# Kernel optimization log

Measured on AMD Instinct MI355X. Metric: run time of the kernel, lower is better.

Reference implementation:

```python
import jax, jax.numpy as jnp
import numpy as np

HEADS = 4


def rel_to_abs(x):
    """Convert relative logits [..., L, 2L-1] to absolute [..., L, L].
    out[..., i, j] = x[..., i, j - i + L - 1]."""
    L = x.shape[-2]
    idx = jnp.arange(L)[None, :] - jnp.arange(L)[:, None] + (L - 1)  # [L, L]
    idx = jnp.broadcast_to(idx, x.shape[:-1] + (L,))
    return jnp.take_along_axis(x, idx, axis=-1)


def setup_inputs() -> dict:
    key = jax.random.key(0)
    ks = jax.random.split(key, 5)
    b, c, h, w = 2, 256, 64, 64
    dh = c // HEADS
    return {
        "x": jax.random.normal(ks[0], (b, c, h, w), jnp.float32),
        "w_qkv": jax.random.normal(ks[1], (3 * c, c), jnp.float32) / np.float32(np.sqrt(c)),
        "w_out": jax.random.normal(ks[2], (c, c), jnp.float32) / np.float32(np.sqrt(c)),
        "rel_height": jax.random.normal(ks[3], (2 * h - 1, dh), jnp.float32),
        "rel_width": jax.random.normal(ks[4], (2 * w - 1, dh), jnp.float32),
    }


def reference(x, w_qkv, w_out, rel_height, rel_width):
    b, c, h, w = x.shape
    dh = c // HEADS
    N = h * w
    scale = dh ** -0.5

    # 1x1 conv == per-pixel matmul over channels
    qkv = jnp.einsum('bchw,oc->bohw', x, w_qkv)  # [b, 3c, h, w]
    q, k, v = jnp.split(qkv, 3, axis=1)

    def to_heads(t):  # [b, c, h, w] -> [b, H, N, dh]
        return t.reshape(b, HEADS, dh, N).transpose(0, 1, 3, 2)

    q = to_heads(q) * scale
    k = to_heads(k)
    v = to_heads(v)

    # content-content scores over spatial positions
    content = jnp.einsum('bnid,bnjd->bnij', q, k)  # [b, H, N, N]

    q5 = q.reshape(b, HEADS, h, w, dh)  # [b, H, x, y, dh]
    # width relative logits: [b,H,x,y,2w-1] -> abs -> [b,H,x,y,jw]
    rw = rel_to_abs(jnp.einsum('bnxyd,rd->bnxyr', q5, rel_width))
    # height relative logits on transposed spatial: [b,H,y,x,2h-1] -> [b,H,y,x,jh]
    rh = rel_to_abs(jnp.einsum('bnyxd,rd->bnyxr', q5.transpose(0, 1, 3, 2, 4), rel_height))

    logits = content.reshape(b, HEADS, h, w, h, w)
    logits = logits + rw[:, :, :, :, None, :]  # broadcast width bias over target height jh
    logits = logits + rh.transpose(0, 1, 3, 2, 4)[:, :, :, :, :, None]  # [b,H,x,y,jh] over jw

    attn = jax.nn.softmax(logits.reshape(b, HEADS, N, N), axis=-1)
    out = jnp.einsum('bnij,bnjd->bnid', attn, v)  # [b, H, N, dh]
    out = out.transpose(0, 1, 3, 2).reshape(b, c, h, w)
    out = jnp.einsum('bchw,oc->bohw', out, w_out)  # 1x1 out projection
    return out + x
```

## Files before the change

kernel.cpp:

```cpp
#include <hip/hip_runtime.h>

typedef unsigned short u16;
typedef unsigned int u32;
typedef __bf16 bf16x8 __attribute__((ext_vector_type(8)));
typedef __bf16 bf16x2 __attribute__((ext_vector_type(2)));
typedef float f32x4 __attribute__((ext_vector_type(4)));
typedef float f32x2 __attribute__((ext_vector_type(2)));
typedef u32 u32x4 __attribute__((ext_vector_type(4)));
typedef u32 u32x2 __attribute__((ext_vector_type(2)));
typedef short s16x4 __attribute__((ext_vector_type(4)));

#define DEVI __device__ __forceinline__

#if defined(__has_builtin)
#if __has_builtin(__builtin_amdgcn_exp2f)
#define EXP2F(x) __builtin_amdgcn_exp2f(x)
#endif
#endif
#ifndef EXP2F
#define EXP2F(x) exp2f(x)
#endif

#define MFMA16(a, b, c) __builtin_amdgcn_mfma_f32_16x16x32_bf16(a, b, c, 0, 0, 0)
#define MFMA1K(a, b, c) __builtin_amdgcn_mfma_f32_16x16x16bf16_1k(a, b, c, 0, 0, 0)

DEVI u16 f2bf(float f) {
    u32 u = __builtin_bit_cast(u32, f);
    u = (u + 0x7FFFu + ((u >> 16) & 1u)) >> 16;
    return (u16)u;
}
DEVI float bf2f(u16 h) {
    u32 u = ((u32)h) << 16;
    return __builtin_bit_cast(float, u);
}
DEVI float bfhi(u32 u) { return __builtin_bit_cast(float, u & 0xFFFF0000u); }
DEVI float bflo(u32 u) { return __builtin_bit_cast(float, u << 16); }
DEVI bf16x8 bc8(u32x4 u) { return __builtin_bit_cast(bf16x8, u); }
DEVI u32 pack2(float a, float b) {
    f32x2 v = {a, b};
    bf16x2 h = __builtin_convertvector(v, bf16x2);
    return __builtin_bit_cast(u32, h);
}

#define QSCALE 0.18033688011112042f

__global__ __launch_bounds__(256) void k_prep(const float* __restrict__ x,
                                              const float* __restrict__ wq,
                                              const float* __restrict__ wo,
                                              const float* __restrict__ relh,
                                              const float* __restrict__ relw,
                                              u16* __restrict__ xt, u16* __restrict__ wqb,
                                              u16* __restrict__ wob, u16* __restrict__ relhb,
                                              u16* __restrict__ relwb) {
    int bid = blockIdx.x;
    int t = threadIdx.x;
    if (bid < 512) {
        int pm = bid & 63, cm = (bid >> 6) & 3, b = bid >> 8;
        int p0 = pm * 64, c0 = cm * 64;
        __shared__ float tile[64][65];
#pragma unroll
        for (int it = 0; it < 16; ++it) {
            int idx = it * 256 + t;
            int cl = idx >> 6, pl = idx & 63;
            tile[cl][pl] = x[((size_t)(b * 256 + c0 + cl)) * 4096 + p0 + pl];
        }
        __syncthreads();
#pragma unroll
        for (int it = 0; it < 16; ++it) {
            int idx = it * 256 + t;
            int pl = idx >> 6, cl = idx & 63;
            xt[((size_t)(b * 4096 + p0 + pl)) * 256 + c0 + cl] = f2bf(tile[cl][pl]);
        }
    } else {
        int i0 = (bid - 512) * 256 + t;
#pragma unroll
        for (int i = i0; i < 196608; i += 65536) wqb[i] = f2bf(wq[i]);
        if (i0 < 65536) wob[i0] = f2bf(wo[i0]);
        if (i0 < 8192) {
            relhb[i0] = (i0 < 8128) ? f2bf(relh[i0]) : (u16)0;
            relwb[i0] = (i0 < 8128) ? f2bf(relw[i0]) : (u16)0;
        }
    }
}

__global__ __launch_bounds__(256) void k_qkv(const u16* __restrict__ xt, const u16* __restrict__ wqb,
                                             const u16* __restrict__ relwb,
                                             const u16* __restrict__ relhb,
                                             u16* __restrict__ q, u16* __restrict__ k,
                                             u16* __restrict__ vt, u16* __restrict__ Wabs,
                                             u16* __restrict__ Habs) {
    int pm = blockIdx.x, on = blockIdx.y, b = blockIdx.z;
    int p0 = pm * 64, o0 = on * 64;
    __shared__ __align__(16) u16 Bt[64 * 264];
    int t = threadIdx.x;
    int wv = t >> 6, l = t & 63, quad = l >> 4, li = l & 15;

    u32x4 areg[8];
    const u32x4* arow = (const u32x4*)(xt + ((size_t)(b * 4096 + p0 + wv * 16 + li)) * 256);
#pragma unroll
    for (int kc = 0; kc < 8; ++kc) areg[kc] = arow[kc * 4 + quad];

    {
        int row = t >> 2, c0 = (t & 3) * 64;
        const u32x4* g = (const u32x4*)(wqb + (size_t)(o0 + row) * 256 + c0);
        u32x4* s = (u32x4*)(Bt + row * 264 + c0);
#pragma unroll
        for (int kk = 0; kk < 8; ++kk) s[kk] = g[kk];
    }
    __syncthreads();

    f32x4 acc[4] = {{0, 0, 0, 0}, {0, 0, 0, 0}, {0, 0, 0, 0}, {0, 0, 0, 0}};
#pragma unroll
    for (int kc = 0; kc < 8; ++kc) {
        bf16x8 a = bc8(areg[kc]);
#pragma unroll
        for (int ct = 0; ct < 4; ++ct) {
            bf16x8 bb = bc8(*(const u32x4*)(Bt + (ct * 16 + li) * 264 + kc * 32 + quad * 8));
            acc[ct] = MFMA16(a, bb, acc[ct]);
        }
    }

    int tensor = on >> 2, head = on & 3;
    if (tensor == 2) {
        __syncthreads();
        u16* T = Bt;
#pragma unroll
        for (int ct = 0; ct < 4; ++ct)
#pragma unroll
            for (int r = 0; r < 4; ++r)
                T[(ct * 16 + li) * 72 + wv * 16 + quad * 4 + r] = f2bf(acc[ct][r]);
        __syncthreads();
        int dr = t >> 2, pc = (t & 3) * 16;
        u32x4* g = (u32x4*)(vt + ((size_t)((b * 4 + head) * 64 + dr)) * 4096 + p0 + pc);
        const u32x4* s2 = (const u32x4*)(T + dr * 72 + pc);
        g[0] = s2[0];
        g[1] = s2[1];
    } else {
        u16* outp = (tensor == 0) ? q : k;
        float sc = (tensor == 0) ? QSCALE : 1.0f;
#pragma unroll
        for (int ct = 0; ct < 4; ++ct)
#pragma unroll
            for (int r = 0; r < 4; ++r) {
                int p = p0 + wv * 16 + quad * 4 + r;
                int d = ct * 16 + li;
                outp[((size_t)((b * 4 + head) * 4096 + p)) * 64 + d] = f2bf(acc[ct][r] * sc);
            }
        if (tensor == 0) {
            int bh = b * 4 + head;
            u16* T = Bt;
            u16* Ls = Bt + 64 * 72;
            __syncthreads();
#pragma unroll
            for (int ct = 0; ct < 4; ++ct)
#pragma unroll
                for (int r = 0; r < 4; ++r)
                    T[(wv * 16 + quad * 4 + r) * 72 + ct * 16 + li] = f2bf(acc[ct][r] * QSCALE);
            {
                int row = t >> 1, half = t & 1;
                const u32x4* g2 = (const u32x4*)(relwb + row * 64 + half * 32);
                u32x4* s2 = (u32x4*)(Ls + row * 72 + half * 32);
#pragma unroll
                for (int kk = 0; kk < 4; ++kk) s2[kk] = g2[kk];
            }
            __syncthreads();
            u32x4 aq2[2];
            aq2[0] = *(const u32x4*)(T + (wv * 16 + li) * 72 + quad * 8);
            aq2[1] = *(const u32x4*)(T + (wv * 16 + li) * 72 + 32 + quad * 8);

            f32x4 acc2[8];
#pragma unroll
            for (int ct = 0; ct < 8; ++ct) acc2[ct] = (f32x4){0.f, 0.f, 0.f, 0.f};
#pragma unroll
            for (int kc = 0; kc < 2; ++kc) {
                bf16x8 a = bc8(aq2[kc]);
#pragma unroll
                for (int ct = 0; ct < 8; ++ct) {
                    bf16x8 bb = bc8(*(const u32x4*)(Ls + (ct * 16 + li) * 72 + kc * 32 + quad * 8));
                    acc2[ct] = MFMA16(a, bb, acc2[ct]);
                }
            }
#pragma unroll
            for (int ct = 0; ct < 8; ++ct)
#pragma unroll
                for (int r = 0; r < 4; ++r) {
                    int row = wv * 16 + quad * 4 + r;
                    int j = (ct * 16 + li) - 63 + row;
                    if (j >= 0 && j < 64)
                        Wabs[((size_t)(bh * 4096 + p0 + row)) * 64 + j] = f2bf(acc2[ct][r]);
                }
            __syncthreads();
            {
                int row = t >> 1, half = t & 1;
                const u32x4* g2 = (const u32x4*)(relhb + row * 64 + half * 32);
                u32x4* s2 = (u32x4*)(Ls + row * 72 + half * 32);
#pragma unroll
                for (int kk = 0; kk < 4; ++kk) s2[kk] = g2[kk];
            }
            __syncthreads();
#pragma unroll
            for (int ct = 0; ct < 8; ++ct) acc2[ct] = (f32x4){0.f, 0.f, 0.f, 0.f};
#pragma unroll
            for (int kc = 0; kc < 2; ++kc) {
                bf16x8 a = bc8(aq2[kc]);
#pragma unroll
                for (int ct = 0; ct < 8; ++ct) {
                    bf16x8 bb = bc8(*(const u32x4*)(Ls + (ct * 16 + li) * 72 + kc * 32 + quad * 8));
                    acc2[ct] = MFMA16(a, bb, acc2[ct]);
                }
            }
#pragma unroll
            for (int ct = 0; ct < 8; ++ct)
#pragma unroll
                for (int r = 0; r < 4; ++r) {
                    int row = wv * 16 + quad * 4 + r;
                    int j = (ct * 16 + li) - 63 + pm;
                    if (j >= 0 && j < 64)
                        Habs[((size_t)(bh * 4096 + p0 + row)) * 64 + j] = f2bf(acc2[ct][r]);
                }
        }
    }
}

__global__ __launch_bounds__(256, 2) void k_flash(const u16* __restrict__ q,
                                                  const u16* __restrict__ kg,
                                                  const u16* __restrict__ vt,
                                                  const u16* __restrict__ Wabs,
                                                  const u16* __restrict__ Habs,
                                                  u16* __restrict__ OP,
                                                  float* __restrict__ LS) {
    int pm = blockIdx.x, bh = blockIdx.y, ks = blockIdx.z;
    int p0 = pm * 128;
    __shared__ __align__(16) u16 Kt[2][64 * 72];
    __shared__ __align__(16) u16 Vl[2][64 * 72];
    __shared__ __align__(16) u16 Hl[128 * 24];
    int t = threadIdx.x, wv = t >> 6, l = t & 63, quad = l >> 4, li = l & 15;
    int rbase = wv * 32;

    u32x4 aq[2][2];
#pragma unroll
    for (int rs = 0; rs < 2; ++rs) {
        const u32x4* qrow =
            (const u32x4*)(q + ((size_t)(bh * 4096 + p0 + rbase + rs * 16 + li)) * 64);
        aq[rs][0] = qrow[quad];
        aq[rs][1] = qrow[4 + quad];
    }

    f32x4 wb4[2][4];
#pragma unroll
    for (int rs = 0; rs < 2; ++rs)
#pragma unroll
        for (int ct = 0; ct < 4; ++ct) {
            const u32* wp = (const u32*)(Wabs +
                                         ((size_t)(bh * 4096 + p0 + rbase + rs * 16 + li)) * 64 +
                                         ct * 16 + quad * 4);
            u32 lo = wp[0], hi = wp[1];
            wb4[rs][ct] = (f32x4){bflo(lo), bfhi(lo), bflo(hi), bfhi(hi)};
        }

    {
        int row = t >> 1, half = t & 1;
        const u32x4* g =
            (const u32x4*)(Habs + ((size_t)(bh * 4096 + p0 + row)) * 64 + ks * 16 + half * 8);
        *(u32x4*)(Hl + row * 24 + half * 8) = g[0];
    }

    int srow = t >> 2, scc = (t & 3) * 16;
    {
        int j0 = ks * 1024;
        const u32x4* gk = (const u32x4*)(kg + ((size_t)(bh * 4096 + j0 + srow)) * 64 + scc);
        u32x4* sk = (u32x4*)(Kt[0] + srow * 72 + scc);
        sk[0] = gk[0];
        sk[1] = gk[1];
        const u32x4* gv = (const u32x4*)(vt + ((size_t)(bh * 64 + srow)) * 4096 + j0 + scc);
        u32x4* sv = (u32x4*)(Vl[0] + srow * 72 + scc);
        sv[0] = gv[0];
        sv[1] = gv[1];
    }

    f32x4 oacc[2][5];
#pragma unroll
    for (int rs = 0; rs < 2; ++rs)
#pragma unroll
        for (int ct = 0; ct < 5; ++ct) oacc[rs][ct] = (f32x4){0.f, 0.f, 0.f, 0.f};

    const s16x4 ones = {(short)0x3F80, (short)0x3F80, (short)0x3F80, (short)0x3F80};

    u32x4 kreg[2], vreg[2];
    for (int kt = 0; kt < 16; ++kt) {
        __syncthreads();
        int cur = kt & 1;
        const u16* Kc = Kt[cur];
        const u16* Vc = Vl[cur];
        if (kt < 15) {
            int j0 = (ks * 16 + kt + 1) * 64;
            const u32x4* gk = (const u32x4*)(kg + ((size_t)(bh * 4096 + j0 + srow)) * 64 + scc);
            kreg[0] = gk[0];
            kreg[1] = gk[1];
            const u32x4* gv = (const u32x4*)(vt + ((size_t)(bh * 64 + srow)) * 4096 + j0 + scc);
            vreg[0] = gv[0];
            vreg[1] = gv[1];
        }

        float hh0 = bf2f(Hl[(rbase + li) * 24 + kt]);
        float hh1 = bf2f(Hl[(rbase + 16 + li) * 24 + kt]);
        f32x4 s[2][4];
#pragma unroll
        for (int ct = 0; ct < 4; ++ct) {
            s[0][ct] = wb4[0][ct] + hh0;
            s[1][ct] = wb4[1][ct] + hh1;
        }
#pragma unroll
        for (int kc = 0; kc < 2; ++kc) {
            bf16x8 b0 = bc8(aq[0][kc]), b1 = bc8(aq[1][kc]);
#pragma unroll
            for (int ct = 0; ct < 4; ++ct) {
                bf16x8 af = bc8(*(const u32x4*)(Kc + (ct * 16 + li) * 72 + kc * 32 + quad * 8));
                s[0][ct] = MFMA16(af, b0, s[0][ct]);
                s[1][ct] = MFMA16(af, b1, s[1][ct]);
            }
        }

        s16x4 pf[2][4];
#pragma unroll
        for (int rs = 0; rs < 2; ++rs)
#pragma unroll
            for (int ct = 0; ct < 4; ++ct) {
                u32x2 pp;
                pp.x = pack2(EXP2F(s[rs][ct][0]), EXP2F(s[rs][ct][1]));
                pp.y = pack2(EXP2F(s[rs][ct][2]), EXP2F(s[rs][ct][3]));
                pf[rs][ct] = __builtin_bit_cast(s16x4, pp);
            }

#pragma unroll
        for (int jt = 0; jt < 4; ++jt) {
            s16x4 a0 = pf[0][jt], a1 = pf[1][jt];
#pragma unroll
            for (int dt = 0; dt < 4; ++dt) {
                s16x4 bv = __builtin_bit_cast(
                    s16x4, *(const u32x2*)(Vc + (dt * 16 + li) * 72 + jt * 16 + quad * 4));
                oacc[0][dt] = MFMA1K(a0, bv, oacc[0][dt]);
                oacc[1][dt] = MFMA1K(a1, bv, oacc[1][dt]);
            }
            oacc[0][4] = MFMA1K(a0, ones, oacc[0][4]);
            oacc[1][4] = MFMA1K(a1, ones, oacc[1][4]);
        }

        if (kt < 15) {
            u32x4* sk = (u32x4*)(Kt[cur ^ 1] + srow * 72 + scc);
            sk[0] = kreg[0];
            sk[1] = kreg[1];
            u32x4* sv = (u32x4*)(Vl[cur ^ 1] + srow * 72 + scc);
            sv[0] = vreg[0];
            sv[1] = vreg[1];
        }
    }

#pragma unroll
    for (int rs = 0; rs < 2; ++rs) {
#pragma unroll
        for (int ct = 0; ct < 4; ++ct)
#pragma unroll
            for (int r = 0; r < 4; ++r) {
                int p = p0 + rbase + rs * 16 + quad * 4 + r;
                OP[((size_t)((ks * 8 + bh) * 4096 + p)) * 64 + ct * 16 + li] =
                    f2bf(oacc[rs][ct][r]);
            }
        if (li == 0) {
#pragma unroll
            for (int r = 0; r < 4; ++r) {
                int p = p0 + rbase + rs * 16 + quad * 4 + r;
                LS[(size_t)(ks * 8 + bh) * 4096 + p] = oacc[rs][4][r];
            }
        }
    }
}

__global__ __launch_bounds__(256) void k_out2(const u16* __restrict__ wob,
                                              const u16* __restrict__ OP,
                                              const float* __restrict__ LS,
                                              const float* __restrict__ x,
                                              float* __restrict__ out) {
    int pm = blockIdx.x, b = blockIdx.y, com = blockIdx.z;
    int p0 = pm * 64;
    __shared__ __align__(16) u16 Bt[64 * 264];
    int t = threadIdx.x, wv = t >> 6, l = t & 63, quad = l >> 4, li = l & 15;

    {
        int row = t >> 2, head = t & 3;
        int bh = b * 4 + head;
        int p = p0 + row;
        const u32x4* op[4];
        float lsum = 0.f;
#pragma unroll
        for (int s2 = 0; s2 < 4; ++s2) {
            op[s2] = (const u32x4*)(OP + ((size_t)((s2 * 8 + bh) * 4096 + p)) * 64);
            lsum += LS[(size_t)(s2 * 8 + bh) * 4096 + p];
        }
        float linv = 1.0f / lsum;
        u16* dst = Bt + row * 264 + head * 64;
#pragma unroll
        for (int kk = 0; kk < 8; ++kk) {
            u32x4 a = op[0][kk], c = op[1][kk], e = op[2][kk], f = op[3][kk];
            u32x4 pk;
            pk.x = pack2((bflo(a.x) + bflo(c.x) + bflo(e.x) + bflo(f.x)) * linv,
                         (bfhi(a.x) + bfhi(c.x) + bfhi(e.x) + bfhi(f.x)) * linv);
            pk.y = pack2((bflo(a.y) + bflo(c.y) + bflo(e.y) + bflo(f.y)) * linv,
                         (bfhi(a.y) + bfhi(c.y) + bfhi(e.y) + bfhi(f.y)) * linv);
            pk.z = pack2((bflo(a.z) + bflo(c.z) + bflo(e.z) + bflo(f.z)) * linv,
                         (bfhi(a.z) + bfhi(c.z) + bfhi(e.z) + bfhi(f.z)) * linv);
            pk.w = pack2((bflo(a.w) + bflo(c.w) + bflo(e.w) + bflo(f.w)) * linv,
                         (bfhi(a.w) + bfhi(c.w) + bfhi(e.w) + bfhi(f.w)) * linv);
            *(u32x4*)(dst + kk * 8) = pk;
        }
    }
    __syncthreads();

    int co0 = com * 64;
    f32x4 acc[4] = {{0, 0, 0, 0}, {0, 0, 0, 0}, {0, 0, 0, 0}, {0, 0, 0, 0}};
    const u32x4* arow = (const u32x4*)(wob + (size_t)(co0 + wv * 16 + li) * 256);
#pragma unroll
    for (int kc = 0; kc < 8; ++kc) {
        bf16x8 a = bc8(arow[kc * 4 + quad]);
#pragma unroll
        for (int ct = 0; ct < 4; ++ct) {
            bf16x8 bb = bc8(*(const u32x4*)(Bt + (ct * 16 + li) * 264 + kc * 32 + quad * 8));
            acc[ct] = MFMA16(a, bb, acc[ct]);
        }
    }
#pragma unroll
    for (int ct = 0; ct < 4; ++ct)
#pragma unroll
        for (int r = 0; r < 4; ++r) {
            size_t idx =
                ((size_t)(b * 256 + co0 + wv * 16 + quad * 4 + r)) * 4096 + p0 + ct * 16 + li;
            out[idx] = acc[ct][r] + x[idx];
        }
}

extern "C" void kernel_launch(void* const* d_in, const int* in_sizes, int n_in, void* d_out,
                              int out_size, void* d_ws, size_t ws_size, hipStream_t stream) {
    const float* x = (const float*)d_in[0];
    const float* wqkv = (const float*)d_in[1];
    const float* wout = (const float*)d_in[2];
    const float* relh = (const float*)d_in[3];
    const float* relw = (const float*)d_in[4];
    float* out = (float*)d_out;
    char* ws = (char*)d_ws;

    u16* xt = (u16*)(ws + 0);
    u16* wqb = (u16*)(ws + 4194304);
    u16* wob = (u16*)(ws + 4587520);
    u16* relwb = (u16*)(ws + 4718592);
    u16* relhb = (u16*)(ws + 4734976);
    u16* qb = (u16*)(ws + 4751360);
    u16* kb = (u16*)(ws + 8945664);
    u16* vtb = (u16*)(ws + 13139968);
    u16* Wabs = (u16*)(ws + 17334272);
    u16* Habs = (u16*)(ws + 21528576);
    u16* OPart = (u16*)(ws + 25722880);
    float* LSum = (float*)(ws + 0);

    k_prep<<<768, 256, 0, stream>>>(x, wqkv, wout, relh, relw, xt, wqb, wob, relhb, relwb);
    k_qkv<<<dim3(64, 12, 2), 256, 0, stream>>>(xt, wqb, relwb, relhb, qb, kb, vtb, Wabs, Habs);
    k_flash<<<dim3(32, 8, 4), 256, 0, stream>>>(qb, kb, vtb, Wabs, Habs, OPart, LSum);
    k_out2<<<dim3(64, 2, 4), 256, 0, stream>>>(wob, OPart, LSum, x, out);
}
```

Before: 153.6 us.

## Use direct global-to-LDS loads, transpose Habs layout, raise flash occupancy, merge out tiles

k_qkv now stages the weight tile with global_load_lds and an XOR/rotation swizzle instead of padded register copies. Habs is written transposed so k_flash can prefetch per-key-tile height biases straight into registers and drop its LDS staging buffer. k_flash launch bounds are raised to 4 blocks per SM. k_out2 computes two output-channel tiles per block, halving the grid and the repeated OP reduction. Risks: the strided transposed Habs writes are uncoalesced, and the higher occupancy may cause register spills.

After: 170.0 us. 1.11x slower.

```diff
diff --git a/kernel.cpp b/kernel.cpp
--- a/kernel.cpp
+++ b/kernel.cpp
@@ -23,6 +23,13 @@
 
 #define MFMA16(a, b, c) __builtin_amdgcn_mfma_f32_16x16x32_bf16(a, b, c, 0, 0, 0)
 #define MFMA1K(a, b, c) __builtin_amdgcn_mfma_f32_16x16x16bf16_1k(a, b, c, 0, 0, 0)
+
+typedef __attribute__((address_space(1))) u32 gu32;
+typedef __attribute__((address_space(3))) u32 lu32;
+DEVI void gll16(const u16* g, u16* l) {
+    __builtin_amdgcn_global_load_lds((const gu32*)g, (lu32*)l, 16, 0, 0);
+}
+#define WAIT_VM0() __builtin_amdgcn_s_waitcnt(0x0f70)
 
 DEVI u16 f2bf(float f) {
     u32 u = __builtin_bit_cast(u32, f);
@@ -88,10 +95,10 @@
                                              const u16* __restrict__ relhb,
                                              u16* __restrict__ q, u16* __restrict__ k,
                                              u16* __restrict__ vt, u16* __restrict__ Wabs,
-                                             u16* __restrict__ Habs) {
+                                             u16* __restrict__ HabsT) {
     int pm = blockIdx.x, on = blockIdx.y, b = blockIdx.z;
     int p0 = pm * 64, o0 = on * 64;
-    __shared__ __align__(16) u16 Bt[64 * 264];
+    __shared__ __align__(16) u16 Sm[64 * 256];
     int t = threadIdx.x;
     int wv = t >> 6, l = t & 63, quad = l >> 4, li = l & 15;
 
@@ -101,12 +108,15 @@
     for (int kc = 0; kc < 8; ++kc) areg[kc] = arow[kc * 4 + quad];
 
     {
-        int row = t >> 2, c0 = (t & 3) * 64;
-        const u32x4* g = (const u32x4*)(wqb + (size_t)(o0 + row) * 256 + c0);
-        u32x4* s = (u32x4*)(Bt + row * 264 + c0);
-#pragma unroll
-        for (int kk = 0; kk < 8; ++kk) s[kk] = g[kk];
-    }
+        int pc = l & 31;
+#pragma unroll
+        for (int i = 0; i < 8; ++i) {
+            int r = wv * 16 + i * 2 + (l >> 5);
+            gll16(wqb + (size_t)(o0 + r) * 256 + ((pc + r) & 31) * 8,
+                  Sm + (wv * 16 + i * 2) * 256);
+        }
+    }
+    WAIT_VM0();
     __syncthreads();
 
     f32x4 acc[4] = {{0, 0, 0, 0}, {0, 0, 0, 0}, {0, 0, 0, 0}, {0, 0, 0, 0}};
@@ -115,7 +125,8 @@
         bf16x8 a = bc8(areg[kc]);
 #pragma unroll
         for (int ct = 0; ct < 4; ++ct) {
-            bf16x8 bb = bc8(*(const u32x4*)(Bt + (ct * 16 + li) * 264 + kc * 32 + quad * 8));
+            bf16x8 bb = bc8(*(const u32x4*)(Sm + (ct * 16 + li) * 256 +
+                                            (((kc * 4 + quad) - (ct * 16 + li)) & 31) * 8));
             acc[ct] = MFMA16(a, bb, acc[ct]);
         }
     }
@@ -123,7 +134,7 @@
     int tensor = on >> 2, head = on & 3;
     if (tensor == 2) {
         __syncthreads();
-        u16* T = Bt;
+        u16* T = Sm;
 #pragma unroll
         for (int ct = 0; ct < 4; ++ct)
 #pragma unroll
@@ -148,8 +159,8 @@
             }
         if (tensor == 0) {
             int bh = b * 4 + head;
-            u16* T = Bt;
-            u16* Ls = Bt + 64 * 72;
+            u16* T = Sm;
+            u16* Ls = Sm + 64 * 72;
             __syncthreads();
 #pragma unroll
             for (int ct = 0; ct < 4; ++ct)
@@ -216,24 +227,23 @@
                     int row = wv * 16 + quad * 4 + r;
                     int j = (ct * 16 + li) - 63 + pm;
                     if (j >= 0 && j < 64)
-                        Habs[((size_t)(bh * 4096 + p0 + row)) * 64 + j] = f2bf(acc2[ct][r]);
+                        HabsT[((size_t)(bh * 64 + j)) * 4096 + p0 + row] = f2bf(acc2[ct][r]);
                 }
         }
     }
 }
 
-__global__ __launch_bounds__(256, 2) void k_flash(const u16* __restrict__ q,
+__global__ __launch_bounds__(256, 4) void k_flash(const u16* __restrict__ q,
                                                   const u16* __restrict__ kg,
                                                   const u16* __restrict__ vt,
                                                   const u16* __restrict__ Wabs,
-                                                  const u16* __restrict__ Habs,
+                                                  const u16* __restrict__ HabsT,
                                                   u16* __restrict__ OP,
                                                   float* __restrict__ LS) {
     int pm = blockIdx.x, bh = blockIdx.y, ks = blockIdx.z;
     int p0 = pm * 128;
     __shared__ __align__(16) u16 Kt[2][64 * 72];
     __shared__ __align__(16) u16 Vl[2][64 * 72];
-    __shared__ __align__(16) u16 Hl[128 * 24];
     int t = threadIdx.x, wv = t >> 6, l = t & 63, quad = l >> 4, li = l & 15;
     int rbase = wv * 32;
 
@@ -258,12 +268,7 @@
             wb4[rs][ct] = (f32x4){bflo(lo), bfhi(lo), bflo(hi), bfhi(hi)};
         }
 
-    {
-        int row = t >> 1, half = t & 1;
-        const u32x4* g =
-            (const u32x4*)(Habs + ((size_t)(bh * 4096 + p0 + row)) * 64 + ks * 16 + half * 8);
-        *(u32x4*)(Hl + row * 24 + half * 8) = g[0];
-    }
+    const u16* hbase = HabsT + ((size_t)(bh * 64 + ks * 16)) * 4096 + p0 + rbase;
 
     int srow = t >> 2, scc = (t & 3) * 16;
     {
@@ -277,6 +282,8 @@
         sv[0] = gv[0];
         sv[1] = gv[1];
     }
+    u16 hc0 = hbase[li];
+    u16 hc1 = hbase[16 + li];
 
     f32x4 oacc[2][5];
 #pragma unroll
@@ -287,6 +294,7 @@
     const s16x4 ones = {(short)0x3F80, (short)0x3F80, (short)0x3F80, (short)0x3F80};
 
     u32x4 kreg[2], vreg[2];
+    u16 hn0, hn1;
     for (int kt = 0; kt < 16; ++kt) {
         __syncthreads();
         int cur = kt & 1;
@@ -300,10 +308,12 @@
             const u32x4* gv = (const u32x4*)(vt + ((size_t)(bh * 64 + srow)) * 4096 + j0 + scc);
             vreg[0] = gv[0];
             vreg[1] = gv[1];
-        }
-
-        float hh0 = bf2f(Hl[(rbase + li) * 24 + kt]);
-        float hh1 = bf2f(Hl[(rbase + 16 + li) * 24 + kt]);
+            hn0 = hbase[(size_t)(kt + 1) * 4096 + li];
+            hn1 = hbase[(size_t)(kt + 1) * 4096 + 16 + li];
+        }
+
+        float hh0 = bf2f(hc0);
+        float hh1 = bf2f(hc1);
         f32x4 s[2][4];
 #pragma unroll
         for (int ct = 0; ct < 4; ++ct) {
@@ -353,6 +363,8 @@
             u32x4* sv = (u32x4*)(Vl[cur ^ 1] + srow * 72 + scc);
             sv[0] = vreg[0];
             sv[1] = vreg[1];
+            hc0 = hn0;
+            hc1 = hn1;
         }
     }
 
@@ -381,7 +393,7 @@
                                               const float* __restrict__ LS,
                                               const float* __restrict__ x,
                                               float* __restrict__ out) {
-    int pm = blockIdx.x, b = blockIdx.y, com = blockIdx.z;
+    int pm = blockIdx.x, b = blockIdx.y, coh = blockIdx.z;
     int p0 = pm * 64;
     __shared__ __align__(16) u16 Bt[64 * 264];
     int t = threadIdx.x, wv = t >> 6, l = t & 63, quad = l >> 4, li = l & 15;
@@ -416,26 +428,30 @@
     }
     __syncthreads();
 
-    int co0 = com * 64;
-    f32x4 acc[4] = {{0, 0, 0, 0}, {0, 0, 0, 0}, {0, 0, 0, 0}, {0, 0, 0, 0}};
-    const u32x4* arow = (const u32x4*)(wob + (size_t)(co0 + wv * 16 + li) * 256);
-#pragma unroll
-    for (int kc = 0; kc < 8; ++kc) {
-        bf16x8 a = bc8(arow[kc * 4 + quad]);
-#pragma unroll
-        for (int ct = 0; ct < 4; ++ct) {
-            bf16x8 bb = bc8(*(const u32x4*)(Bt + (ct * 16 + li) * 264 + kc * 32 + quad * 8));
-            acc[ct] = MFMA16(a, bb, acc[ct]);
-        }
-    }
-#pragma unroll
-    for (int ct = 0; ct < 4; ++ct)
-#pragma unroll
-        for (int r = 0; r < 4; ++r) {
-            size_t idx =
-                ((size_t)(b * 256 + co0 + wv * 16 + quad * 4 + r)) * 4096 + p0 + ct * 16 + li;
-            out[idx] = acc[ct][r] + x[idx];
-        }
+#pragma unroll
+    for (int ci = 0; ci < 2; ++ci) {
+        int com = coh * 2 + ci;
+        int co0 = com * 64;
+        f32x4 acc[4] = {{0, 0, 0, 0}, {0, 0, 0, 0}, {0, 0, 0, 0}, {0, 0, 0, 0}};
+        const u32x4* arow = (const u32x4*)(wob + (size_t)(co0 + wv * 16 + li) * 256);
+#pragma unroll
+        for (int kc = 0; kc < 8; ++kc) {
+            bf16x8 a = bc8(arow[kc * 4 + quad]);
+#pragma unroll
+            for (int ct = 0; ct < 4; ++ct) {
+                bf16x8 bb = bc8(*(const u32x4*)(Bt + (ct * 16 + li) * 264 + kc * 32 + quad * 8));
+                acc[ct] = MFMA16(a, bb, acc[ct]);
+            }
+        }
+#pragma unroll
+        for (int ct = 0; ct < 4; ++ct)
+#pragma unroll
+            for (int r = 0; r < 4; ++r) {
+                size_t idx =
+                    ((size_t)(b * 256 + co0 + wv * 16 + quad * 4 + r)) * 4096 + p0 + ct * 16 + li;
+                out[idx] = acc[ct][r] + x[idx];
+            }
+    }
 }
 
 extern "C" void kernel_launch(void* const* d_in, const int* in_sizes, int n_in, void* d_out,
@@ -457,12 +473,12 @@
     u16* kb = (u16*)(ws + 8945664);
     u16* vtb = (u16*)(ws + 13139968);
     u16* Wabs = (u16*)(ws + 17334272);
-    u16* Habs = (u16*)(ws + 21528576);
+    u16* HabsT = (u16*)(ws + 21528576);
     u16* OPart = (u16*)(ws + 25722880);
     float* LSum = (float*)(ws + 0);
 
     k_prep<<<768, 256, 0, stream>>>(x, wqkv, wout, relh, relw, xt, wqb, wob, relhb, relwb);
-    k_qkv<<<dim3(64, 12, 2), 256, 0, stream>>>(xt, wqb, relwb, relhb, qb, kb, vtb, Wabs, Habs);
-    k_flash<<<dim3(32, 8, 4), 256, 0, stream>>>(qb, kb, vtb, Wabs, Habs, OPart, LSum);
-    k_out2<<<dim3(64, 2, 4), 256, 0, stream>>>(wob, OPart, LSum, x, out);
-}
+    k_qkv<<<dim3(64, 12, 2), 256, 0, stream>>>(xt, wqb, relwb, relhb, qb, kb, vtb, Wabs, HabsT);
+    k_flash<<<dim3(32, 8, 4), 256, 0, stream>>>(qb, kb, vtb, Wabs, HabsT, OPart, LSum);
+    k_out2<<<dim3(64, 2, 2), 256, 0, stream>>>(wob, OPart, LSum, x, out);
+}
```
